# Kernel optimization log

Hardware: AMD Instinct MI355X
Metric: run time of the kernel (lower is better)

The kernel has to match this reference:

```python
import jax, jax.numpy as jnp
import numpy as np

N_NODES = 100_000
N_EDGES = 1_600_000
IN_DIM = 512
HID = 128
OUT_DIM = 40


def setup_inputs() -> dict:
    key = jax.random.key(0)
    ks = jax.random.split(key, 12)
    s = 0.05  # small init scale
    x = jax.random.normal(ks[0], (N_NODES, IN_DIM), dtype=jnp.float32)
    edge_index = jax.random.randint(ks[1], (2, N_EDGES), 0, N_NODES, dtype=jnp.int64)
    W1 = jax.random.normal(ks[2], (IN_DIM, HID), dtype=jnp.float32) * s
    b1 = jnp.zeros((HID,), jnp.float32)
    Wg0 = jax.random.normal(ks[3], (HID, HID), dtype=jnp.float32) * s
    bg0 = jnp.zeros((HID,), jnp.float32)
    Wg1 = jax.random.normal(ks[4], (HID, HID), dtype=jnp.float32) * s
    bg1 = jnp.zeros((HID,), jnp.float32)
    W2 = jax.random.normal(ks[5], (HID, OUT_DIM), dtype=jnp.float32) * s
    b2 = jnp.zeros((OUT_DIM,), jnp.float32)
    return dict(x=x, edge_index=edge_index, W1=W1, b1=b1, Wg0=Wg0, bg0=bg0,
                Wg1=Wg1, bg1=bg1, W2=W2, b2=b2)


def _gcn_norm(edge_index, num_nodes, dtype):
    # PyG GCNConv default: add self-loops, symmetric normalization D^-1/2 A D^-1/2.
    loops = jnp.arange(num_nodes, dtype=edge_index.dtype)
    src = jnp.concatenate([edge_index[0], loops])  # [E+N]
    dst = jnp.concatenate([edge_index[1], loops])
    deg = jax.ops.segment_sum(jnp.ones(dst.shape, dtype), dst, num_segments=num_nodes)
    dinv = jnp.where(deg > 0, jax.lax.rsqrt(deg), jnp.zeros((), dtype))
    norm = dinv[src] * dinv[dst]  # [E+N]
    return src, dst, norm


def _gcn_conv(h, src, dst, norm, W, b, num_nodes):
    # out[dst] += norm * (h @ W)[src]; then bias
    hw = h @ W                              # [N, HID]
    msg = hw[src] * norm[:, None]           # gather + scale  [E+N, HID]
    agg = jax.ops.segment_sum(msg, dst, num_segments=num_nodes)  # scatter-add
    return agg + b


def reference(x, edge_index, W1, b1, Wg0, bg0, Wg1, bg1, W2, b2):
    n = x.shape[0]
    src, dst, norm = _gcn_norm(edge_index, n, x.dtype)
    h = jax.nn.relu(x @ W1 + b1)  # dropout is identity in eval mode
    for W, b in ((Wg0, bg0), (Wg1, bg1)):
        h = jax.nn.relu(_gcn_conv(h, src, dst, norm, W, b, n))
    logits = h @ W2 + b2
    return jax.nn.log_softmax(logits, axis=1)
```

## Files before the change

kernel.cpp:

```cpp
#include <hip/hip_runtime.h>
#include <hip/hip_bf16.h>
#include <cstdint>

#define HID 128

typedef short s16x8 __attribute__((ext_vector_type(8)));
typedef float f32x4 __attribute__((ext_vector_type(4)));

static inline size_t align_up(size_t x, size_t a) { return (x + a - 1) & ~(a - 1); }

__device__ inline ushort f2bf(float f) {
  uint u = __float_as_uint(f);
  u += 0x7FFFu + ((u >> 16) & 1u);
  return (ushort)(u >> 16);
}
__device__ inline uint pk2bf(float lo, float hi) {
  __hip_bfloat162 h = __float22bfloat162_rn(float2{lo, hi});
  return *reinterpret_cast<uint*>(&h);
}
__device__ inline float bf2f_lo(uint v) { return __uint_as_float(v << 16); }
__device__ inline float bf2f_hi(uint v) { return __uint_as_float(v & 0xFFFF0000u); }

__global__ void detect_i64_kernel(const unsigned int* __restrict__ p, int nwords,
                                  int* __restrict__ flag) {
  __shared__ int any;
  if (threadIdx.x == 0) any = 0;
  __syncthreads();
  for (int i = threadIdx.x; i < 1024; i += blockDim.x) {
    int w = 2 * i + 1;
    if (w < nwords && p[w] != 0u) atomicOr(&any, 1);
  }
  __syncthreads();
  if (threadIdx.x == 0) *flag = (any == 0) ? 1 : 0;
}

__global__ void extract_count_kernel(const void* __restrict__ ei, const int* __restrict__ flag,
                                     int E, int2* __restrict__ sd, int* __restrict__ cnt) {
  int e = blockIdx.x * blockDim.x + threadIdx.x;
  if (e >= E) return;
  int s, d;
  if (*flag) {
    const long long* p = (const long long*)ei;
    s = (int)p[e];
    d = (int)p[(size_t)E + e];
  } else {
    const int* p = (const int*)ei;
    s = p[e];
    d = p[(size_t)E + e];
  }
  sd[e] = int2{s, d};
  atomicAdd(&cnt[d], 1);
}

__global__ void dinv_kernel(const int* __restrict__ cnt, float* __restrict__ dinv, int N) {
  int i = blockIdx.x * blockDim.x + threadIdx.x;
  if (i >= N) return;
  dinv[i] = rsqrtf((float)(cnt[i] + 1));
}

__global__ __launch_bounds__(1024) void scan_local_kernel(const int* __restrict__ cnt,
    int* __restrict__ off, int* __restrict__ bsum, int N) {
  __shared__ int buf[1024];
  int tid = threadIdx.x;
  int i = blockIdx.x * 1024 + tid;
  int v = (i < N) ? cnt[i] : 0;
  buf[tid] = v;
  __syncthreads();
  #pragma unroll
  for (int s = 1; s < 1024; s <<= 1) {
    int t = (tid >= s) ? buf[tid - s] : 0;
    __syncthreads();
    buf[tid] += t;
    __syncthreads();
  }
  if (i < N) off[i] = buf[tid] - v;
  if (tid == 1023) bsum[blockIdx.x] = buf[1023];
}

__global__ __launch_bounds__(128) void scan_bsum_kernel(const int* __restrict__ bsum, int nb,
    int* __restrict__ boff, int* __restrict__ offN) {
  __shared__ int b[128];
  int tid = threadIdx.x;
  int v = (tid < nb) ? bsum[tid] : 0;
  b[tid] = v;
  __syncthreads();
  #pragma unroll
  for (int s = 1; s < 128; s <<= 1) {
    int t = (tid >= s) ? b[tid - s] : 0;
    __syncthreads();
    b[tid] += t;
    __syncthreads();
  }
  if (tid < nb) boff[tid] = b[tid] - v;
  if (tid == 127) *offN = b[127];
}

__global__ void scan_add_kernel(int* __restrict__ off, const int* __restrict__ boff,
                                int* __restrict__ cursor, int N) {
  int i = blockIdx.x * blockDim.x + threadIdx.x;
  if (i >= N) return;
  int o = off[i] + boff[i >> 10];
  off[i] = o;
  cursor[i] = o;
}

__global__ void fill_kernel(const int2* __restrict__ sd, const float* __restrict__ dinv,
                            int* __restrict__ cursor, int2* __restrict__ csr, int E) {
  int e = blockIdx.x * blockDim.x + threadIdx.x;
  if (e >= E) return;
  int2 p = sd[e];
  int pos = atomicAdd(&cursor[p.y], 1);
  float nm = dinv[p.x] * dinv[p.y];
  csr[pos] = int2{p.x, __float_as_int(nm)};
}

__global__ void convert_w_kernel(const float* __restrict__ W, ushort* __restrict__ Wt,
                                 int K, int KP) {
  int id = blockIdx.x * blockDim.x + threadIdx.x;
  if (id >= K * 128) return;
  int c = id & 127;
  int k = id >> 7;
  Wt[(size_t)c * KP + k] = f2bf(W[id]);
}

__global__ void convert_w2_kernel(const float* __restrict__ W2, ushort* __restrict__ Wt) {
  int id = blockIdx.x * blockDim.x + threadIdx.x;
  if (id >= 48 * 128) return;
  int c = id >> 7;
  int k = id & 127;
  Wt[(size_t)c * 128 + k] = (c < 40) ? f2bf(W2[(size_t)k * 40 + c]) : (ushort)0;
}

template <int K, bool AF32, bool BIAS_RELU, int WAVES>
__global__ __launch_bounds__(WAVES * 64, (WAVES == 16) ? 4 : 16 / WAVES)
void gemm_lds_kernel(
    const void* __restrict__ Ap, const ushort* __restrict__ Wtp,
    const float* __restrict__ bias, ushort* __restrict__ outp,
    int M, int rowsPerBlock) {
  constexpr int KP = K + 8;
  extern __shared__ __align__(16) ushort lB[];
  const int tid = threadIdx.x;

  const int rowStart = blockIdx.x * rowsPerBlock;
  if (rowStart >= M) return;
  const int rowEnd = min(M, rowStart + rowsPerBlock);

  constexpr int TOTC = 128 * KP / 8;
  const s16x8* Wt8 = (const s16x8*)Wtp;
  for (int i = tid; i < TOTC; i += WAVES * 64) ((s16x8*)lB)[i] = Wt8[i];
  __syncthreads();

  const int w = tid >> 6;
  const int l = tid & 63;
  const int l15 = l & 15;
  const int kg = l >> 4;

  const ushort* Ab = (const ushort*)Ap;
  const float* Af = (const float*)Ap;

  for (int base = rowStart + w * 16; base < rowEnd; base += WAVES * 16) {
    int row = base + l15;
    if (row >= M) row = M - 1;

    f32x4 acc[8];
    #pragma unroll
    for (int c = 0; c < 8; ++c) acc[c] = f32x4{0.f, 0.f, 0.f, 0.f};

    if constexpr (AF32) {
      const float* ar = &Af[(size_t)row * K + kg * 8];
      float4 p0 = *(const float4*)ar;
      float4 p1 = *(const float4*)(ar + 4);
      #pragma unroll 4
      for (int k0 = 0; k0 < K; k0 += 32) {
        float4 c0 = p0, c1 = p1;
        if (k0 + 32 < K) {
          p0 = *(const float4*)(ar + k0 + 32);
          p1 = *(const float4*)(ar + k0 + 36);
        }
        uint4 u;
        u.x = pk2bf(c0.x, c0.y);
        u.y = pk2bf(c0.z, c0.w);
        u.z = pk2bf(c1.x, c1.y);
        u.w = pk2bf(c1.z, c1.w);
        s16x8 af = *reinterpret_cast<s16x8*>(&u);
        #pragma unroll
        for (int c = 0; c < 8; ++c) {
          s16x8 bfr = *(const s16x8*)&lB[(16 * c + l15) * KP + k0 + kg * 8];
          acc[c] = __builtin_amdgcn_mfma_f32_16x16x32_bf16(af, bfr, acc[c], 0, 0, 0);
        }
      }
    } else {
      s16x8 afs[K / 32];
      #pragma unroll
      for (int k0 = 0; k0 < K; k0 += 32)
        afs[k0 / 32] = *(const s16x8*)&Ab[(size_t)row * K + k0 + kg * 8];
      #pragma unroll
      for (int k0 = 0; k0 < K; k0 += 32) {
        #pragma unroll
        for (int c = 0; c < 8; ++c) {
          s16x8 bfr = *(const s16x8*)&lB[(16 * c + l15) * KP + k0 + kg * 8];
          acc[c] = __builtin_amdgcn_mfma_f32_16x16x32_bf16(afs[k0 / 32], bfr, acc[c], 0, 0, 0);
        }
      }
    }

    #pragma unroll
    for (int c = 0; c < 8; ++c) {
      float b = 0.f;
      if constexpr (BIAS_RELU) b = bias[16 * c + l15];
      #pragma unroll
      for (int v = 0; v < 4; ++v) {
        int r = base + kg * 4 + v;
        if (r < M) {
          float val = acc[c][v];
          if constexpr (BIAS_RELU) val = fmaxf(val + b, 0.f);
          outp[(size_t)r * 128 + 16 * c + l15] = f2bf(val);
        }
      }
    }
  }
}

__global__ __launch_bounds__(256) void aggregate_bf16_kernel(const ushort* __restrict__ hw,
    const int* __restrict__ off, const int2* __restrict__ csr,
    const float* __restrict__ dinv, const float* __restrict__ bias,
    ushort* __restrict__ out, int N) {
  int wid = (blockIdx.x * blockDim.x + threadIdx.x) >> 6;
  int lane = threadIdx.x & 63;
  if (wid >= N) return;
  const uint* hw4 = (const uint*)hw;
  int beg = off[wid], end = off[wid + 1];
  float ax = 0.f, ay = 0.f;
  int j = beg;
  int n8 = beg + ((end - beg) & ~7);
  for (; j < n8; j += 8) {
    int2 c0 = csr[j];     int2 c1 = csr[j + 1];
    int2 c2 = csr[j + 2]; int2 c3 = csr[j + 3];
    int2 c4 = csr[j + 4]; int2 c5 = csr[j + 5];
    int2 c6 = csr[j + 6]; int2 c7 = csr[j + 7];
    uint v0 = hw4[(size_t)c0.x * 64 + lane];
    uint v1 = hw4[(size_t)c1.x * 64 + lane];
    uint v2 = hw4[(size_t)c2.x * 64 + lane];
    uint v3 = hw4[(size_t)c3.x * 64 + lane];
    uint v4 = hw4[(size_t)c4.x * 64 + lane];
    uint v5 = hw4[(size_t)c5.x * 64 + lane];
    uint v6 = hw4[(size_t)c6.x * 64 + lane];
    uint v7 = hw4[(size_t)c7.x * 64 + lane];
    float n0 = __int_as_float(c0.y), n1 = __int_as_float(c1.y);
    float n2 = __int_as_float(c2.y), n3 = __int_as_float(c3.y);
    float n4 = __int_as_float(c4.y), n5 = __int_as_float(c5.y);
    float n6 = __int_as_float(c6.y), n7 = __int_as_float(c7.y);
    ax = fmaf(n0, bf2f_lo(v0), ax); ay = fmaf(n0, bf2f_hi(v0), ay);
    ax = fmaf(n1, bf2f_lo(v1), ax); ay = fmaf(n1, bf2f_hi(v1), ay);
    ax = fmaf(n2, bf2f_lo(v2), ax); ay = fmaf(n2, bf2f_hi(v2), ay);
    ax = fmaf(n3, bf2f_lo(v3), ax); ay = fmaf(n3, bf2f_hi(v3), ay);
    ax = fmaf(n4, bf2f_lo(v4), ax); ay = fmaf(n4, bf2f_hi(v4), ay);
    ax = fmaf(n5, bf2f_lo(v5), ax); ay = fmaf(n5, bf2f_hi(v5), ay);
    ax = fmaf(n6, bf2f_lo(v6), ax); ay = fmaf(n6, bf2f_hi(v6), ay);
    ax = fmaf(n7, bf2f_lo(v7), ax); ay = fmaf(n7, bf2f_hi(v7), ay);
  }
  if (j + 4 <= end) {
    int2 c0 = csr[j];     int2 c1 = csr[j + 1];
    int2 c2 = csr[j + 2]; int2 c3 = csr[j + 3];
    uint v0 = hw4[(size_t)c0.x * 64 + lane];
    uint v1 = hw4[(size_t)c1.x * 64 + lane];
    uint v2 = hw4[(size_t)c2.x * 64 + lane];
    uint v3 = hw4[(size_t)c3.x * 64 + lane];
    float n0 = __int_as_float(c0.y), n1 = __int_as_float(c1.y);
    float n2 = __int_as_float(c2.y), n3 = __int_as_float(c3.y);
    ax = fmaf(n0, bf2f_lo(v0), ax); ay = fmaf(n0, bf2f_hi(v0), ay);
    ax = fmaf(n1, bf2f_lo(v1), ax); ay = fmaf(n1, bf2f_hi(v1), ay);
    ax = fmaf(n2, bf2f_lo(v2), ax); ay = fmaf(n2, bf2f_hi(v2), ay);
    ax = fmaf(n3, bf2f_lo(v3), ax); ay = fmaf(n3, bf2f_hi(v3), ay);
    j += 4;
  }
  for (; j < end; ++j) {
    int2 c = csr[j];
    float nm = __int_as_float(c.y);
    uint v = hw4[(size_t)c.x * 64 + lane];
    ax = fmaf(nm, bf2f_lo(v), ax);
    ay = fmaf(nm, bf2f_hi(v), ay);
  }
  float di = dinv[wid];
  float snm = di * di;
  uint v = hw4[(size_t)wid * 64 + lane];
  ax = fmaf(snm, bf2f_lo(v), ax);
  ay = fmaf(snm, bf2f_hi(v), ay);
  float2 b = ((const float2*)bias)[lane];
  float ox = fmaxf(ax + b.x, 0.f);
  float oy = fmaxf(ay + b.y, 0.f);
  ((uint*)out)[(size_t)wid * 64 + lane] = pk2bf(ox, oy);
}

__global__ __launch_bounds__(256) void final_mfma_kernel(const ushort* __restrict__ h,
    const ushort* __restrict__ W2t, const float* __restrict__ b2,
    float* __restrict__ out, int M) {
  const int tid = threadIdx.x;
  const int w = tid >> 6;
  const int l = tid & 63;
  const int l15 = l & 15;
  const int kg = l >> 4;
  const int base = (blockIdx.x * 4 + w) * 16;
  if (base >= M) return;
  int row = base + l15;
  if (row >= M) row = M - 1;

  f32x4 acc[3];
  #pragma unroll
  for (int c = 0; c < 3; ++c) acc[c] = f32x4{0.f, 0.f, 0.f, 0.f};

  #pragma unroll
  for (int k0 = 0; k0 < 128; k0 += 32) {
    s16x8 af = *(const s16x8*)&h[(size_t)row * 128 + k0 + kg * 8];
    #pragma unroll
    for (int c = 0; c < 3; ++c) {
      s16x8 bfr = *(const s16x8*)&W2t[(size_t)(16 * c + l15) * 128 + k0 + kg * 8];
      acc[c] = __builtin_amdgcn_mfma_f32_16x16x32_bf16(af, bfr, acc[c], 0, 0, 0);
    }
  }

  float bv0 = b2[l15];
  float bv1 = b2[16 + l15];
  float bv2 = (l15 < 8) ? b2[32 + l15] : 0.f;

  #pragma unroll
  for (int v = 0; v < 4; ++v) {
    float l0 = acc[0][v] + bv0;
    float l1 = acc[1][v] + bv1;
    float l2 = (l15 < 8) ? (acc[2][v] + bv2) : -1e30f;
    float pm = fmaxf(fmaxf(l0, l1), l2);
    #pragma unroll
    for (int sh = 8; sh > 0; sh >>= 1) pm = fmaxf(pm, __shfl_xor(pm, sh));
    float es = expf(l0 - pm) + expf(l1 - pm) + ((l15 < 8) ? expf(l2 - pm) : 0.f);
    #pragma unroll
    for (int sh = 8; sh > 0; sh >>= 1) es += __shfl_xor(es, sh);
    float lse = pm + logf(es);
    int r = base + kg * 4 + v;
    if (r < M) {
      out[(size_t)r * 40 + l15] = l0 - lse;
      out[(size_t)r * 40 + 16 + l15] = l1 - lse;
      if (l15 < 8) out[(size_t)r * 40 + 32 + l15] = l2 - lse;
    }
  }
}

extern "C" void kernel_launch(void* const* d_in, const int* in_sizes, int n_in,
                              void* d_out, int out_size, void* d_ws, size_t ws_size,
                              hipStream_t stream) {
  const float* x   = (const float*)d_in[0];
  const void*  ei  = d_in[1];
  const float* W1  = (const float*)d_in[2];
  const float* b1  = (const float*)d_in[3];
  const float* Wg0 = (const float*)d_in[4];
  const float* bg0 = (const float*)d_in[5];
  const float* Wg1 = (const float*)d_in[6];
  const float* bg1 = (const float*)d_in[7];
  const float* W2  = (const float*)d_in[8];
  const float* b2  = (const float*)d_in[9];
  float* out = (float*)d_out;

  const int N = in_sizes[0] / 512;
  const int E = in_sizes[1] / 2;

  char* wsb = (char*)d_ws;
  size_t o = 0;
  auto alloc = [&](size_t bytes) -> void* {
    void* p = wsb + o;
    o = align_up(o + bytes, 256);
    return p;
  };
  int*    flag    = (int*)alloc(4);
  int2*   sd      = (int2*)alloc((size_t)E * 8);
  int*    cnt     = (int*)alloc((size_t)N * 4);
  float*  dinv    = (float*)alloc((size_t)N * 4);
  int*    off     = (int*)alloc((size_t)(N + 1) * 4);
  int*    cursor  = (int*)alloc((size_t)N * 4);
  int*    bsum    = (int*)alloc(128 * 4);
  int*    boff    = (int*)alloc(128 * 4);
  int2*   csr     = (int2*)alloc((size_t)E * 8);
  ushort* W1t     = (ushort*)alloc((size_t)128 * 520 * 2);
  ushort* Wg0t    = (ushort*)alloc((size_t)128 * 136 * 2);
  ushort* Wg1t    = (ushort*)alloc((size_t)128 * 136 * 2);
  ushort* W2t     = (ushort*)alloc((size_t)48 * 128 * 2);
  ushort* hb1     = (ushort*)alloc((size_t)N * HID * 2);
  ushort* hb2     = (ushort*)alloc((size_t)N * HID * 2);
  (void)ws_size; (void)n_in; (void)out_size;

  const int tpb = 256;
  const int ebl = (E + tpb - 1) / tpb;
  const int nbl = (N + tpb - 1) / tpb;

  detect_i64_kernel<<<1, 256, 0, stream>>>((const unsigned int*)ei, 2 * E, flag);
  hipMemsetAsync(cnt, 0, (size_t)N * 4, stream);
  extract_count_kernel<<<ebl, tpb, 0, stream>>>(ei, flag, E, sd, cnt);
  dinv_kernel<<<nbl, tpb, 0, stream>>>(cnt, dinv, N);
  const int nsb = (N + 1023) / 1024;
  scan_local_kernel<<<nsb, 1024, 0, stream>>>(cnt, off, bsum, N);
  scan_bsum_kernel<<<1, 128, 0, stream>>>(bsum, nsb, boff, off + N);
  scan_add_kernel<<<nbl, tpb, 0, stream>>>(off, boff, cursor, N);
  fill_kernel<<<ebl, tpb, 0, stream>>>(sd, dinv, cursor, csr, E);

  convert_w_kernel<<<(512 * 128 + 255) / 256, 256, 0, stream>>>(W1, W1t, 512, 520);
  convert_w_kernel<<<(128 * 128 + 255) / 256, 256, 0, stream>>>(Wg0, Wg0t, 128, 136);
  convert_w_kernel<<<(128 * 128 + 255) / 256, 256, 0, stream>>>(Wg1, Wg1t, 128, 136);
  convert_w2_kernel<<<(48 * 128 + 255) / 256, 256, 0, stream>>>(W2, W2t);

  const size_t lds512 = (size_t)128 * 520 * 2;
  const size_t lds128 = (size_t)128 * 136 * 2;
  static bool attr_done = false;
  if (!attr_done) {
    (void)hipFuncSetAttribute(
        reinterpret_cast<const void*>(&gemm_lds_kernel<512, true, true, 16>),
        hipFuncAttributeMaxDynamicSharedMemorySize, (int)lds512);
    attr_done = true;
  }

  int rpb512 = (N + 255) / 256;
  rpb512 = (rpb512 + 15) & ~15;
  const int grid512 = (N + rpb512 - 1) / rpb512;
  const int rpb128 = 128;
  const int grid128 = (N + rpb128 - 1) / rpb128;
  const int abl = (N * 64 + tpb - 1) / tpb;
  const int fbl = (N + 63) / 64;

  gemm_lds_kernel<512, true, true, 16><<<grid512, 1024, lds512, stream>>>(
      x, W1t, b1, hb1, N, rpb512);

  gemm_lds_kernel<128, false, false, 4><<<grid128, 256, lds128, stream>>>(
      hb1, Wg0t, nullptr, hb2, N, rpb128);
  aggregate_bf16_kernel<<<abl, tpb, 0, stream>>>(hb2, off, csr, dinv, bg0, hb1, N);

  gemm_lds_kernel<128, false, false, 4><<<grid128, 256, lds128, stream>>>(
      hb1, Wg1t, nullptr, hb2, N, rpb128);
  aggregate_bf16_kernel<<<abl, tpb, 0, stream>>>(hb2, off, csr, dinv, bg1, hb1, N);

  final_mfma_kernel<<<fbl, 256, 0, stream>>>(hb1, W2t, b2, out, N);
}
```

Measured before the change: 474.1 us.

## Drop edge staging buffer, fuse dinv into scan, deepen A prefetch in GEMM

The count kernel now reads only destination indices, and the fill kernel re-reads source and destination straight from edge_index, so the intermediate int2 sd buffer is no longer written and read back. The degree-inverse computation moves into the local scan kernel, which removes one launch. Separately, the f32-input GEMM prefetches two 32-wide K chunks per iteration and fully unrolls, aiming to hide more global load latency at the cost of higher register pressure. Re-reading 64-bit edge data in the fill kernel adds read traffic in exchange for skipping the sd write and read.

New measurement: 754.3 us. 59.1% more time.

```diff
diff --git a/kernel.cpp b/kernel.cpp
--- a/kernel.cpp
+++ b/kernel.cpp
@@ -34,32 +34,18 @@
   if (threadIdx.x == 0) *flag = (any == 0) ? 1 : 0;
 }
 
-__global__ void extract_count_kernel(const void* __restrict__ ei, const int* __restrict__ flag,
-                                     int E, int2* __restrict__ sd, int* __restrict__ cnt) {
+__global__ void count_kernel(const void* __restrict__ ei, const int* __restrict__ flag,
+                             int E, int* __restrict__ cnt) {
   int e = blockIdx.x * blockDim.x + threadIdx.x;
   if (e >= E) return;
-  int s, d;
-  if (*flag) {
-    const long long* p = (const long long*)ei;
-    s = (int)p[e];
-    d = (int)p[(size_t)E + e];
-  } else {
-    const int* p = (const int*)ei;
-    s = p[e];
-    d = p[(size_t)E + e];
-  }
-  sd[e] = int2{s, d};
+  int d;
+  if (*flag) d = (int)((const long long*)ei)[(size_t)E + e];
+  else       d = ((const int*)ei)[(size_t)E + e];
   atomicAdd(&cnt[d], 1);
 }
 
-__global__ void dinv_kernel(const int* __restrict__ cnt, float* __restrict__ dinv, int N) {
-  int i = blockIdx.x * blockDim.x + threadIdx.x;
-  if (i >= N) return;
-  dinv[i] = rsqrtf((float)(cnt[i] + 1));
-}
-
 __global__ __launch_bounds__(1024) void scan_local_kernel(const int* __restrict__ cnt,
-    int* __restrict__ off, int* __restrict__ bsum, int N) {
+    int* __restrict__ off, int* __restrict__ bsum, float* __restrict__ dinv, int N) {
   __shared__ int buf[1024];
   int tid = threadIdx.x;
   int i = blockIdx.x * 1024 + tid;
@@ -73,7 +59,10 @@
     buf[tid] += t;
     __syncthreads();
   }
-  if (i < N) off[i] = buf[tid] - v;
+  if (i < N) {
+    off[i] = buf[tid] - v;
+    dinv[i] = rsqrtf((float)(v + 1));
+  }
   if (tid == 1023) bsum[blockIdx.x] = buf[1023];
 }
 
@@ -104,14 +93,24 @@
   cursor[i] = o;
 }
 
-__global__ void fill_kernel(const int2* __restrict__ sd, const float* __restrict__ dinv,
-                            int* __restrict__ cursor, int2* __restrict__ csr, int E) {
+__global__ void fill_kernel(const void* __restrict__ ei, const int* __restrict__ flag,
+                            const float* __restrict__ dinv, int* __restrict__ cursor,
+                            int2* __restrict__ csr, int E) {
   int e = blockIdx.x * blockDim.x + threadIdx.x;
   if (e >= E) return;
-  int2 p = sd[e];
-  int pos = atomicAdd(&cursor[p.y], 1);
-  float nm = dinv[p.x] * dinv[p.y];
-  csr[pos] = int2{p.x, __float_as_int(nm)};
+  int s, d;
+  if (*flag) {
+    const long long* p = (const long long*)ei;
+    s = (int)p[e];
+    d = (int)p[(size_t)E + e];
+  } else {
+    const int* p = (const int*)ei;
+    s = p[e];
+    d = p[(size_t)E + e];
+  }
+  int pos = atomicAdd(&cursor[d], 1);
+  float nm = dinv[s] * dinv[d];
+  csr[pos] = int2{s, __float_as_int(nm)};
 }
 
 __global__ void convert_w_kernel(const float* __restrict__ W, ushort* __restrict__ Wt,
@@ -168,25 +167,36 @@
 
     if constexpr (AF32) {
       const float* ar = &Af[(size_t)row * K + kg * 8];
-      float4 p0 = *(const float4*)ar;
-      float4 p1 = *(const float4*)(ar + 4);
-      #pragma unroll 4
-      for (int k0 = 0; k0 < K; k0 += 32) {
-        float4 c0 = p0, c1 = p1;
-        if (k0 + 32 < K) {
-          p0 = *(const float4*)(ar + k0 + 32);
-          p1 = *(const float4*)(ar + k0 + 36);
+      f32x4 a0 = *(const f32x4*)(ar);
+      f32x4 a1 = *(const f32x4*)(ar + 4);
+      f32x4 b0 = *(const f32x4*)(ar + 32);
+      f32x4 b1 = *(const f32x4*)(ar + 36);
+      #pragma unroll
+      for (int k0 = 0; k0 < K; k0 += 64) {
+        f32x4 c0 = a0, c1 = a1, d0 = b0, d1 = b1;
+        if (k0 + 64 < K) {
+          a0 = *(const f32x4*)(ar + k0 + 64);
+          a1 = *(const f32x4*)(ar + k0 + 68);
+          b0 = *(const f32x4*)(ar + k0 + 96);
+          b1 = *(const f32x4*)(ar + k0 + 100);
         }
         uint4 u;
-        u.x = pk2bf(c0.x, c0.y);
-        u.y = pk2bf(c0.z, c0.w);
-        u.z = pk2bf(c1.x, c1.y);
-        u.w = pk2bf(c1.z, c1.w);
-        s16x8 af = *reinterpret_cast<s16x8*>(&u);
+        u.x = pk2bf(c0.x, c0.y); u.y = pk2bf(c0.z, c0.w);
+        u.z = pk2bf(c1.x, c1.y); u.w = pk2bf(c1.z, c1.w);
+        s16x8 af0 = *reinterpret_cast<s16x8*>(&u);
         #pragma unroll
         for (int c = 0; c < 8; ++c) {
           s16x8 bfr = *(const s16x8*)&lB[(16 * c + l15) * KP + k0 + kg * 8];
-          acc[c] = __builtin_amdgcn_mfma_f32_16x16x32_bf16(af, bfr, acc[c], 0, 0, 0);
+          acc[c] = __builtin_amdgcn_mfma_f32_16x16x32_bf16(af0, bfr, acc[c], 0, 0, 0);
+        }
+        uint4 u2;
+        u2.x = pk2bf(d0.x, d0.y); u2.y = pk2bf(d0.z, d0.w);
+        u2.z = pk2bf(d1.x, d1.y); u2.w = pk2bf(d1.z, d1.w);
+        s16x8 af1 = *reinterpret_cast<s16x8*>(&u2);
+        #pragma unroll
+        for (int c = 0; c < 8; ++c) {
+          s16x8 bfr = *(const s16x8*)&lB[(16 * c + l15) * KP + k0 + 32 + kg * 8];
+          acc[c] = __builtin_amdgcn_mfma_f32_16x16x32_bf16(af1, bfr, acc[c], 0, 0, 0);
         }
       }
     } else {
@@ -370,7 +380,6 @@
     return p;
   };
   int*    flag    = (int*)alloc(4);
-  int2*   sd      = (int2*)alloc((size_t)E * 8);
   int*    cnt     = (int*)alloc((size_t)N * 4);
   float*  dinv    = (float*)alloc((size_t)N * 4);
   int*    off     = (int*)alloc((size_t)(N + 1) * 4);
@@ -392,13 +401,12 @@
 
   detect_i64_kernel<<<1, 256, 0, stream>>>((const unsigned int*)ei, 2 * E, flag);
   hipMemsetAsync(cnt, 0, (size_t)N * 4, stream);
-  extract_count_kernel<<<ebl, tpb, 0, stream>>>(ei, flag, E, sd, cnt);
-  dinv_kernel<<<nbl, tpb, 0, stream>>>(cnt, dinv, N);
+  count_kernel<<<ebl, tpb, 0, stream>>>(ei, flag, E, cnt);
   const int nsb = (N + 1023) / 1024;
-  scan_local_kernel<<<nsb, 1024, 0, stream>>>(cnt, off, bsum, N);
+  scan_local_kernel<<<nsb, 1024, 0, stream>>>(cnt, off, bsum, dinv, N);
   scan_bsum_kernel<<<1, 128, 0, stream>>>(bsum, nsb, boff, off + N);
   scan_add_kernel<<<nbl, tpb, 0, stream>>>(off, boff, cursor, N);
-  fill_kernel<<<ebl, tpb, 0, stream>>>(sd, dinv, cursor, csr, E);
+  fill_kernel<<<ebl, tpb, 0, stream>>>(ei, flag, dinv, cursor, csr, E);
 
   convert_w_kernel<<<(512 * 128 + 255) / 256, 256, 0, stream>>>(W1, W1t, 512, 520);
   convert_w_kernel<<<(128 * 128 + 255) / 256, 256, 0, stream>>>(Wg0, Wg0t, 128, 136);
```
